# Kernel tuning notes

Hardware: AMD Instinct MI355X
Metric: run time of the kernel (lower is better)

## Reference

```python
import jax, jax.numpy as jnp
import numpy as np

B = 16384          # batch
N_SPARSE = 16      # single-id sparse features
N_VARLEN = 4       # variable-length sparse features
L = 50             # max sequence length per varlen feature
V = 1_000_000      # vocab per table
D = 1              # linear embedding dim (DeepCTR Linear uses dim=1)
INIT_STD = 1e-4
EPS = 1e-8


def setup_inputs() -> dict:
    key = jax.random.key(0)
    k1, k2, k3 = jax.random.split(key, 3)
    X = jax.random.randint(k1, (B, N_SPARSE + N_VARLEN * L), 0, V, dtype=jnp.int32)
    sparse_tables = jax.random.normal(k2, (N_SPARSE, V, D), dtype=jnp.float32) * INIT_STD
    varlen_tables = jax.random.normal(k3, (N_VARLEN, V, D), dtype=jnp.float32) * INIT_STD
    return {"X": X, "sparse_tables": sparse_tables, "varlen_tables": varlen_tables}


def reference(X, sparse_tables, varlen_tables):
    # --- single-id sparse lookups: one gather per table, vectorized over tables ---
    sparse_ids = X[:, :N_SPARSE]                                  # [B, Ns]
    f_idx = jnp.arange(N_SPARSE)[None, :]                          # [1, Ns]
    sparse_emb = sparse_tables[f_idx, sparse_ids]                  # [B, Ns, D]

    # --- varlen lookups + masked mean pooling (mask: id != 0, DeepCTR convention) ---
    varlen_ids = X[:, N_SPARSE:].reshape(B, N_VARLEN, L)           # [B, Nv, L]
    v_idx = jnp.arange(N_VARLEN)[None, :, None]                    # [1, Nv, 1]
    varlen_emb = varlen_tables[v_idx, varlen_ids]                  # [B, Nv, L, D]
    mask = (varlen_ids != 0).astype(varlen_emb.dtype)[..., None]   # [B, Nv, L, 1]
    summed = jnp.sum(varlen_emb * mask, axis=2)                    # [B, Nv, D]
    lengths = jnp.sum(mask, axis=2)                                # [B, Nv, 1]
    pooled = summed / (lengths + EPS)                              # [B, Nv, D]

    # --- concat and flatten, matching torch.flatten(concat_fun(...), start_dim=1) ---
    out = jnp.concatenate([sparse_emb, pooled], axis=1)            # [B, Ns+Nv, D]
    return out.reshape(B, -1)                                      # [B, (Ns+Nv)*D]
```

## Files before the change

### kernel.cpp

```cpp
#include <hip/hip_runtime.h>

#define B 16384
#define N_SPARSE 16
#define N_VARLEN 4
#define L 50
#define V 1000000
#define ROW (N_SPARSE + N_VARLEN * L)
#define OUT_W (N_SPARSE + N_VARLEN)
#define KLANES 8
#define NITER 7

#define VARLEN_BLOCKS 2048
#define SPARSE_BLOCKS 1024

__global__ __launch_bounds__(256) void emb_gather_pool_kernel(
    const int* __restrict__ X,
    const float* __restrict__ sparse_tables,
    const float* __restrict__ varlen_tables,
    float* __restrict__ out)
{
    const int bid = blockIdx.x;
    const int t   = threadIdx.x;

    if (bid < VARLEN_BLOCKS) {
        const int xcd  = bid & 7;
        const int f    = xcd & 3;
        const int half = xcd >> 2;
        const int slot = bid >> 3;
        const int task = t >> 3;
        const int lane = t & (KLANES - 1);
        const int row  = half * (B / 2) + slot * 32 + task;

        const int*   ids = X + row * ROW + N_SPARSE + f * L;
        const float* tab = varlen_tables + (long)f * V;

        int id[NITER];
        #pragma unroll
        for (int k = 0; k < NITER; ++k) {
            const int l = lane + k * KLANES;
            id[k] = (l < L) ? __builtin_nontemporal_load(ids + l) : 0;
        }

        float v[NITER];
        #pragma unroll
        for (int k = 0; k < NITER; ++k) {
            v[k] = tab[id[k]];
        }

        float sum = 0.0f;
        float cnt = 0.0f;
        #pragma unroll
        for (int k = 0; k < NITER; ++k) {
            const float m = (id[k] != 0) ? 1.0f : 0.0f;
            sum = fmaf(m, v[k], sum);
            cnt += m;
        }

        #pragma unroll
        for (int off = 1; off < KLANES; off <<= 1) {
            sum += __shfl_xor(sum, off);
            cnt += __shfl_xor(cnt, off);
        }

        if (lane == 0) {
            __builtin_nontemporal_store(sum / (cnt + 1e-8f),
                                        out + row * OUT_W + N_SPARSE + f);
        }
    } else {
        const int sb  = bid - VARLEN_BLOCKS;
        const int rl  = t >> 4;
        const int j   = t & 15;
        const int row = sb * 16 + rl;

        const int   id = __builtin_nontemporal_load(X + row * ROW + j);
        const float v  = __builtin_nontemporal_load(sparse_tables + (long)j * V + id);
        __builtin_nontemporal_store(v, out + row * OUT_W + j);
    }
}

extern "C" void kernel_launch(void* const* d_in, const int* in_sizes, int n_in,
                              void* d_out, int out_size, void* d_ws, size_t ws_size,
                              hipStream_t stream) {
    const int*   X             = (const int*)  d_in[0];
    const float* sparse_tables = (const float*)d_in[1];
    const float* varlen_tables = (const float*)d_in[2];
    float*       out           = (float*)d_out;

    const int grid  = VARLEN_BLOCKS + SPARSE_BLOCKS;
    const int block = 256;

    emb_gather_pool_kernel<<<grid, block, 0, stream>>>(X, sparse_tables, varlen_tables, out);
}
```

Before: 127.6 us.

## Assign varlen work per physical XCD via hardware XCC id and atomic slot pool

Result: slower. 161.6 us (+26.6%).

```diff
diff --git a/kernel.cpp b/kernel.cpp
--- a/kernel.cpp
+++ b/kernel.cpp
@@ -10,29 +10,50 @@
 #define KLANES 8
 #define NITER 7
 
+#define SPARSE_BLOCKS 1024
 #define VARLEN_BLOCKS 2048
-#define SPARSE_BLOCKS 1024
+#define SLOTS_PER_XCD 256
 
 __global__ __launch_bounds__(256) void emb_gather_pool_kernel(
     const int* __restrict__ X,
     const float* __restrict__ sparse_tables,
     const float* __restrict__ varlen_tables,
-    float* __restrict__ out)
+    float* __restrict__ out,
+    int* __restrict__ xcd_pool)
 {
     const int bid = blockIdx.x;
     const int t   = threadIdx.x;
 
-    if (bid < VARLEN_BLOCKS) {
-        const int xcd  = bid & 7;
-        const int f    = xcd & 3;
-        const int half = xcd >> 2;
-        const int slot = bid >> 3;
+    if (bid < SPARSE_BLOCKS) {
+        const int rl  = t >> 4;
+        const int j   = t & 15;
+        const int row = bid * 16 + rl;
+
+        const int   id = __builtin_nontemporal_load(X + row * ROW + j);
+        const float v  = __builtin_nontemporal_load(sparse_tables + (long)j * V + id);
+        __builtin_nontemporal_store(v, out + row * OUT_W + j);
+        return;
+    }
+
+    unsigned int xcc;
+    asm volatile("s_getreg_b32 %0, hwreg(HW_REG_XCC_ID)" : "=s"(xcc));
+    xcc &= 7;
+    const int f    = xcc & 3;
+    const int half = xcc >> 2;
+    const float* tab = varlen_tables + (long)f * V;
+
+    __shared__ int s_slot;
+    for (;;) {
+        if (t == 0) s_slot = atomicAdd(xcd_pool + xcc, 1);
+        __syncthreads();
+        const int slot = s_slot;
+        __syncthreads();
+        if (slot >= SLOTS_PER_XCD) break;
+
         const int task = t >> 3;
         const int lane = t & (KLANES - 1);
         const int row  = half * (B / 2) + slot * 32 + task;
-
-        const int*   ids = X + row * ROW + N_SPARSE + f * L;
-        const float* tab = varlen_tables + (long)f * V;
+        const int* ids = X + row * ROW + N_SPARSE + f * L;
 
         int id[NITER];
         #pragma unroll
@@ -66,15 +87,6 @@
             __builtin_nontemporal_store(sum / (cnt + 1e-8f),
                                         out + row * OUT_W + N_SPARSE + f);
         }
-    } else {
-        const int sb  = bid - VARLEN_BLOCKS;
-        const int rl  = t >> 4;
-        const int j   = t & 15;
-        const int row = sb * 16 + rl;
-
-        const int   id = __builtin_nontemporal_load(X + row * ROW + j);
-        const float v  = __builtin_nontemporal_load(sparse_tables + (long)j * V + id);
-        __builtin_nontemporal_store(v, out + row * OUT_W + j);
     }
 }
 
@@ -85,9 +97,13 @@
     const float* sparse_tables = (const float*)d_in[1];
     const float* varlen_tables = (const float*)d_in[2];
     float*       out           = (float*)d_out;
+    int*         xcd_pool      = (int*)d_ws;
 
-    const int grid  = VARLEN_BLOCKS + SPARSE_BLOCKS;
+    hipMemsetAsync(xcd_pool, 0, 8 * sizeof(int), stream);
+
+    const int grid  = SPARSE_BLOCKS + VARLEN_BLOCKS;
     const int block = 256;
 
-    emb_gather_pool_kernel<<<grid, block, 0, stream>>>(X, sparse_tables, varlen_tables, out);
+    emb_gather_pool_kernel<<<grid, block, 0, stream>>>(X, sparse_tables, varlen_tables,
+                                                       out, xcd_pool);
 }
```
